# Performance work log

Measured on AMD Instinct MI355X. Metric: run time of the kernel, lower is better.

## Reference

```python
import jax, jax.numpy as jnp
import numpy as np

B, T, C = 2, 2048, 1024
H = 16
HD = C // H  # head_dim = 64


def setup_inputs() -> dict:
    key = jax.random.key(0)
    ks = jax.random.split(key, 5)
    s = 0.02
    return {
        "x": jax.random.normal(ks[0], (B, T, C), dtype=jnp.float32),
        "Wqkv": jax.random.normal(ks[1], (C, 3 * C), dtype=jnp.float32) * s,
        "bqkv": jax.random.normal(ks[2], (3 * C,), dtype=jnp.float32) * s,
        "Wproj": jax.random.normal(ks[3], (C, C), dtype=jnp.float32) * s,
        "bproj": jax.random.normal(ks[4], (C,), dtype=jnp.float32) * s,
    }


def reference(x, Wqkv, bqkv, Wproj, bproj):
    b, t, c = x.shape
    qkv = x @ Wqkv + bqkv  # [B,T,3C]
    q, k, v = jnp.split(qkv, 3, axis=-1)
    # [B,T,C] -> [B,H,T,HD]
    q = q.reshape(b, t, H, HD).transpose(0, 2, 1, 3)
    k = k.reshape(b, t, H, HD).transpose(0, 2, 1, 3)
    v = v.reshape(b, t, H, HD).transpose(0, 2, 1, 3)
    scale = 1.0 / jnp.sqrt(jnp.float32(HD))
    att = jnp.einsum('bhqd,bhkd->bhqk', q, k) * scale  # [B,H,T,T]
    causal = jnp.tril(jnp.ones((t, t), dtype=bool))
    att = jnp.where(causal[None, None], att, jnp.float32(-jnp.inf))
    att = jax.nn.softmax(att, axis=-1)
    y = jnp.einsum('bhqk,bhkd->bhqd', att, v)  # [B,H,T,HD]
    y = y.transpose(0, 2, 1, 3).reshape(b, t, c)
    return y @ Wproj + bproj
```

## Files before the change

### kernel.cpp

```cpp
#include <hip/hip_runtime.h>

typedef unsigned short u16;
typedef __attribute__((ext_vector_type(4))) float f32x4;
typedef __attribute__((ext_vector_type(8))) short short8;

#define AS1 __attribute__((address_space(1)))
#define AS3 __attribute__((address_space(3)))

#define B_  2
#define T_  2048
#define C_  1024
#define H_  16
#define HD_ 64
#define N3C 3072
#define BT_ 4096

__device__ __forceinline__ u16 f2bf(float x) {
    unsigned u = __float_as_uint(x);
    u += 0x7fff + ((u >> 16) & 1);
    return (u16)(u >> 16);
}

__device__ __forceinline__ unsigned cvt_pk_bf16(float a, float b) {
    unsigned r;
    asm("v_cvt_pk_bf16_f32 %0, %1, %2" : "=v"(r) : "v"(a), "v"(b));
    return r;
}

__global__ __launch_bounds__(256)
void conv_all(const float* __restrict__ x, u16* __restrict__ xb,
              const float* __restrict__ Wq, u16* __restrict__ WqT,
              const float* __restrict__ Wp, u16* __restrict__ WpT) {
    __shared__ float tile[64][68];
    const int tid = threadIdx.x;
    const int b = blockIdx.x;
    if (b < 4096) {
        int i = b * 256 + tid;
        float4 f = ((const float4*)x)[i];
        uint2 o;
        o.x = cvt_pk_bf16(f.x, f.y);
        o.y = cvt_pk_bf16(f.z, f.w);
        ((uint2*)xb)[i] = o;
        return;
    }
    const float* W; u16* WT; int N, k0, n0;
    if (b < 4096 + 768) {
        int bb = b - 4096; W = Wq; WT = WqT; N = N3C;
        n0 = (bb % 48) * 64; k0 = (bb / 48) * 64;
    } else {
        int bb = b - 4864; W = Wp; WT = WpT; N = C_;
        n0 = (bb % 16) * 64; k0 = (bb / 16) * 64;
    }
    #pragma unroll
    for (int i = 0; i < 4; ++i) {
        int slot = tid + i * 256;
        int row = slot >> 4, c4 = (slot & 15) * 4;
        *(float4*)&tile[row][c4] = *(const float4*)&W[(size_t)(k0 + row) * N + n0 + c4];
    }
    __syncthreads();
    #pragma unroll
    for (int i = 0; i < 4; ++i) {
        int slot = tid + i * 256;
        int nn = slot >> 4, k4 = (slot & 15) * 4;
        uint2 o;
        o.x = cvt_pk_bf16(tile[k4 + 0][nn], tile[k4 + 1][nn]);
        o.y = cvt_pk_bf16(tile[k4 + 2][nn], tile[k4 + 3][nn]);
        *(uint2*)&WT[(size_t)(n0 + nn) * 1024 + k0 + k4] = o;
    }
}

__device__ __forceinline__ void gemm_core(const u16* __restrict__ A, const u16* __restrict__ BT,
                                          u16* As, u16* Bs,
                                          int m0, int n0, f32x4 (&acc)[4][4]) {
    const int tid = threadIdx.x;
    const int lane = tid & 63, w = tid >> 6;
    const int l15 = lane & 15, quad = lane >> 4;
    const int row0 = (w >> 1) * 64, col0 = (w & 1) * 64;
    const int srow = lane >> 3;
    const int schunk = (lane & 7) ^ srow;

    auto stage = [&](int buf, int k0) {
        #pragma unroll
        for (int j = 0; j < 4; ++j) {
            int rbase = w * 32 + j * 8;
            const u16* ga = A  + (size_t)(m0 + rbase + srow) * 1024 + k0 + schunk * 8;
            const u16* gb = BT + (size_t)(n0 + rbase + srow) * 1024 + k0 + schunk * 8;
            __builtin_amdgcn_global_load_lds((const AS1 void*)ga,
                (AS3 void*)(As + buf * (128 * 64) + rbase * 64), 16, 0, 0);
            __builtin_amdgcn_global_load_lds((const AS1 void*)gb,
                (AS3 void*)(Bs + buf * (128 * 64) + rbase * 64), 16, 0, 0);
        }
    };

    stage(0, 0);
    #pragma unroll
    for (int it = 0; it < 16; ++it) {
        const int cur = it & 1;
        if (it + 1 < 16) {
            stage(cur ^ 1, (it + 1) * 64);
            asm volatile("s_waitcnt vmcnt(8)\n\ts_barrier" ::: "memory");
        } else {
            asm volatile("s_waitcnt vmcnt(0)\n\ts_barrier" ::: "memory");
        }
        const u16* Ac = As + cur * (128 * 64);
        const u16* Bc = Bs + cur * (128 * 64);
        #pragma unroll
        for (int s = 0; s < 2; ++s) {
            short8 a[4], b[4];
            #pragma unroll
            for (int rt = 0; rt < 4; ++rt) {
                int row = row0 + rt * 16 + l15;
                a[rt] = *(const short8*)&Ac[row * 64 + (((s * 4 + quad) ^ (l15 & 7)) * 8)];
            }
            #pragma unroll
            for (int ct = 0; ct < 4; ++ct) {
                int row = col0 + ct * 16 + l15;
                b[ct] = *(const short8*)&Bc[row * 64 + (((s * 4 + quad) ^ (l15 & 7)) * 8)];
            }
            #pragma unroll
            for (int rt = 0; rt < 4; ++rt)
                #pragma unroll
                for (int ct = 0; ct < 4; ++ct)
                    acc[rt][ct] = __builtin_amdgcn_mfma_f32_16x16x32_bf16(a[rt], b[ct], acc[rt][ct], 0, 0, 0);
        }
        asm volatile("s_waitcnt lgkmcnt(0)\n\ts_barrier" ::: "memory");
    }
}

__global__ __launch_bounds__(256)
void qkv_gemm(const u16* __restrict__ A, const u16* __restrict__ BT,
              const float* __restrict__ bias,
              u16* __restrict__ q, u16* __restrict__ k, u16* __restrict__ vT) {
    __shared__ __align__(16) u16 As[2 * 128 * 64];
    __shared__ __align__(16) u16 Bs[2 * 128 * 64];
    const int m0 = blockIdx.y * 128, n0 = blockIdx.x * 128;
    f32x4 acc[4][4] = {};
    gemm_core(A, BT, As, Bs, m0, n0, acc);

    const int tid = threadIdx.x;
    const int lane = tid & 63, w = tid >> 6;
    const int l15 = lane & 15, quad = lane >> 4;
    const int row0 = (w >> 1) * 64, col0 = (w & 1) * 64;
    const int which = n0 >> 10;
    const float QSCALE = 0.125f * 1.4426950408889634f;

    #pragma unroll
    for (int ct = 0; ct < 4; ++ct) {
        int n = n0 + col0 + ct * 16 + l15;
        int nl = n & 1023, h = nl >> 6, d = nl & 63;
        float bv = bias[n];
        #pragma unroll
        for (int rt = 0; rt < 4; ++rt) {
            int mb = m0 + row0 + rt * 16 + quad * 4;
            int bb = mb >> 11, t0 = mb & 2047;
            f32x4 v4 = acc[rt][ct];
            if (which == 0) {
                size_t base = ((size_t)(bb * H_ + h) * T_ + t0) * HD_ + d;
                #pragma unroll
                for (int r = 0; r < 4; ++r)
                    q[base + (size_t)r * HD_] = f2bf((v4[r] + bv) * QSCALE);
            } else if (which == 1) {
                size_t base = ((size_t)(bb * H_ + h) * T_ + t0) * HD_ + d;
                #pragma unroll
                for (int r = 0; r < 4; ++r)
                    k[base + (size_t)r * HD_] = f2bf(v4[r] + bv);
            } else {
                uint2 o;
                o.x = cvt_pk_bf16(v4[0] + bv, v4[1] + bv);
                o.y = cvt_pk_bf16(v4[2] + bv, v4[3] + bv);
                *(uint2*)&vT[((size_t)(bb * H_ + h) * HD_ + d) * T_ + t0] = o;
            }
        }
    }
}

__global__ __launch_bounds__(256, 4)
void attn(const u16* __restrict__ q, const u16* __restrict__ k,
          const u16* __restrict__ vT, u16* __restrict__ y) {
    __shared__ __align__(16) u16 Ks[2 * 64 * 64];
    __shared__ __align__(16) u16 Vs[2 * 64 * 64];
    const int tid = threadIdx.x;
    const int lane = tid & 63, w = tid >> 6;
    const int l15 = lane & 15, quad = lane >> 4;
    const int srow = lane >> 3, schunk = (lane & 7) ^ srow;
    const int idx = blockIdx.x;
    const int bh = idx & 31;
    const int qt = 31 - (idx >> 5);
    const u16* qp = q  + (size_t)bh * T_ * HD_;
    const u16* kp = k  + (size_t)bh * T_ * HD_;
    const u16* vp = vT + (size_t)bh * HD_ * T_;

    const int qrow = qt * 64 + w * 16 + l15;
    short8 qf[2];
    #pragma unroll
    for (int s = 0; s < 2; ++s)
        qf[s] = *(const short8*)&qp[(size_t)qrow * HD_ + s * 32 + quad * 8];

    auto stage = [&](int buf, int kt) {
        const int kb = kt * 64;
        asm volatile("s_waitcnt lgkmcnt(0)" ::: "memory");
        #pragma unroll
        for (int j = 0; j < 2; ++j) {
            int row = w * 16 + j * 8 + srow;
            __builtin_amdgcn_global_load_lds(
                (const AS1 void*)(kp + (size_t)(kb + row) * HD_ + schunk * 8),
                (AS3 void*)(Ks + buf * (64 * 64) + (w * 16 + j * 8) * 64), 16, 0, 0);
            __builtin_amdgcn_global_load_lds(
                (const AS1 void*)(vp + (size_t)row * T_ + kb + schunk * 8),
                (AS3 void*)(Vs + buf * (64 * 64) + (w * 16 + j * 8) * 64), 16, 0, 0);
        }
    };

    f32x4 o[4] = {};
    float l = 0.f;
    stage(0, 0);

    for (int kt = 0; kt <= qt; ++kt) {
        const int kb = kt * 64;
        const int cur = kt & 1;
        if (kt < qt) {
            stage(cur ^ 1, kt + 1);
            asm volatile("s_waitcnt vmcnt(4)\n\ts_barrier" ::: "memory");
        } else {
            asm volatile("s_waitcnt vmcnt(0)\n\ts_barrier" ::: "memory");
        }
        u16* Kc = Ks + cur * (64 * 64);
        const u16* Vc = Vs + cur * (64 * 64);

        short8 ka[4][2], va[4][2];
        #pragma unroll
        for (int ct = 0; ct < 4; ++ct)
            #pragma unroll
            for (int s = 0; s < 2; ++s) {
                int xo = ((s * 4 + quad) ^ (l15 & 7)) * 8;
                ka[ct][s] = *(const short8*)&Kc[(ct * 16 + l15) * 64 + xo];
                va[ct][s] = *(const short8*)&Vc[(ct * 16 + l15) * 64 + xo];
            }
        asm volatile("s_waitcnt lgkmcnt(0)\n\ts_barrier" ::: "memory");

        f32x4 st[4] = {};
        #pragma unroll
        for (int s = 0; s < 2; ++s)
            #pragma unroll
            for (int ct = 0; ct < 4; ++ct)
                st[ct] = __builtin_amdgcn_mfma_f32_16x16x32_bf16(ka[ct][s], qf[s], st[ct], 0, 0, 0);

        float pe[16];
        #pragma unroll
        for (int ct = 0; ct < 4; ++ct)
            #pragma unroll
            for (int r = 0; r < 4; ++r)
                pe[ct * 4 + r] = exp2f(st[ct][r]);
        if (kt == qt) {
            #pragma unroll
            for (int ct = 0; ct < 4; ++ct)
                #pragma unroll
                for (int r = 0; r < 4; ++r)
                    if ((kb + ct * 16 + quad * 4 + r) > qrow) pe[ct * 4 + r] = 0.f;
        }
        float psum = 0.f;
        #pragma unroll
        for (int i = 0; i < 16; ++i) psum += pe[i];
        l += psum;

        u16* Pw = Kc + (w * 16 + l15) * 64;
        #pragma unroll
        for (int ct = 0; ct < 4; ++ct) {
            int chunk = ct * 2 + (quad >> 1);
            int off = ((chunk ^ (l15 & 7)) << 3) + (quad & 1) * 4;
            uint2 pk;
            pk.x = cvt_pk_bf16(pe[ct * 4 + 0], pe[ct * 4 + 1]);
            pk.y = cvt_pk_bf16(pe[ct * 4 + 2], pe[ct * 4 + 3]);
            *(uint2*)&Pw[off] = pk;
        }
        asm volatile("s_waitcnt lgkmcnt(0)" ::: "memory");

        #pragma unroll
        for (int s = 0; s < 2; ++s) {
            short8 pb = *(const short8*)&Pw[(((s * 4 + quad) ^ (l15 & 7)) << 3)];
            #pragma unroll
            for (int n = 0; n < 4; ++n)
                o[n] = __builtin_amdgcn_mfma_f32_16x16x32_bf16(va[n][s], pb, o[n], 0, 0, 0);
        }
    }

    l += __shfl_xor(l, 16); l += __shfl_xor(l, 32);
    const float inv = 1.f / l;
    const int bb = bh >> 4, h = bh & 15;
    #pragma unroll
    for (int n = 0; n < 4; ++n) {
        uint2 pk;
        pk.x = cvt_pk_bf16(o[n][0] * inv, o[n][1] * inv);
        pk.y = cvt_pk_bf16(o[n][2] * inv, o[n][3] * inv);
        *(uint2*)&y[((size_t)(bb * T_ + qrow)) * C_ + h * 64 + n * 16 + quad * 4] = pk;
    }
}

__global__ __launch_bounds__(256, 3)
void proj_gemm(const u16* __restrict__ A, const u16* __restrict__ BT,
               const float* __restrict__ bias, float* __restrict__ out) {
    __shared__ __align__(16) u16 As[2 * 128 * 64];
    __shared__ __align__(16) u16 Bs[2 * 64 * 64];
    const int m0 = blockIdx.y * 128, n0 = blockIdx.x * 64;
    const int tid = threadIdx.x;
    const int lane = tid & 63, w = tid >> 6;
    const int l15 = lane & 15, quad = lane >> 4;
    const int row0 = (w & 1) * 64, col0 = (w >> 1) * 32;
    const int srow = lane >> 3;
    const int schunk = (lane & 7) ^ srow;
    f32x4 acc[4][2] = {};

    auto stage = [&](int buf, int k0) {
        #pragma unroll
        for (int j = 0; j < 4; ++j) {
            int rbase = w * 32 + j * 8;
            const u16* ga = A + (size_t)(m0 + rbase + srow) * 1024 + k0 + schunk * 8;
            __builtin_amdgcn_global_load_lds((const AS1 void*)ga,
                (AS3 void*)(As + buf * (128 * 64) + rbase * 64), 16, 0, 0);
        }
        #pragma unroll
        for (int j = 0; j < 2; ++j) {
            int rbase = w * 16 + j * 8;
            const u16* gb = BT + (size_t)(n0 + rbase + srow) * 1024 + k0 + schunk * 8;
            __builtin_amdgcn_global_load_lds((const AS1 void*)gb,
                (AS3 void*)(Bs + buf * (64 * 64) + rbase * 64), 16, 0, 0);
        }
    };

    stage(0, 0);
    #pragma unroll
    for (int it = 0; it < 16; ++it) {
        const int cur = it & 1;
        if (it + 1 < 16) {
            stage(cur ^ 1, (it + 1) * 64);
            asm volatile("s_waitcnt vmcnt(6)\n\ts_barrier" ::: "memory");
        } else {
            asm volatile("s_waitcnt vmcnt(0)\n\ts_barrier" ::: "memory");
        }
        const u16* Ac = As + cur * (128 * 64);
        const u16* Bc = Bs + cur * (64 * 64);
        #pragma unroll
        for (int s = 0; s < 2; ++s) {
            short8 a[4], b[2];
            #pragma unroll
            for (int rt = 0; rt < 4; ++rt) {
                int row = row0 + rt * 16 + l15;
                a[rt] = *(const short8*)&Ac[row * 64 + (((s * 4 + quad) ^ (l15 & 7)) * 8)];
            }
            #pragma unroll
            for (int ct = 0; ct < 2; ++ct) {
                int row = col0 + ct * 16 + l15;
                b[ct] = *(const short8*)&Bc[row * 64 + (((s * 4 + quad) ^ (l15 & 7)) * 8)];
            }
            #pragma unroll
            for (int rt = 0; rt < 4; ++rt)
                #pragma unroll
                for (int ct = 0; ct < 2; ++ct)
                    acc[rt][ct] = __builtin_amdgcn_mfma_f32_16x16x32_bf16(a[rt], b[ct], acc[rt][ct], 0, 0, 0);
        }
        asm volatile("s_waitcnt lgkmcnt(0)\n\ts_barrier" ::: "memory");
    }

    #pragma unroll
    for (int ct = 0; ct < 2; ++ct) {
        int n = n0 + col0 + ct * 16 + l15;
        float bv = bias[n];
        #pragma unroll
        for (int rt = 0; rt < 4; ++rt) {
            int mb = m0 + row0 + rt * 16 + quad * 4;
            f32x4 v4 = acc[rt][ct];
            #pragma unroll
            for (int r = 0; r < 4; ++r)
                out[(size_t)(mb + r) * 1024 + n] = v4[r] + bv;
        }
    }
}

extern "C" void kernel_launch(void* const* d_in, const int* in_sizes, int n_in,
                              void* d_out, int out_size, void* d_ws, size_t ws_size,
                              hipStream_t stream) {
    const float* x     = (const float*)d_in[0];
    const float* Wqkv  = (const float*)d_in[1];
    const float* bqkv  = (const float*)d_in[2];
    const float* Wproj = (const float*)d_in[3];
    const float* bproj = (const float*)d_in[4];

    u16* xb     = (u16*)d_ws;
    u16* WqkvT  = xb + (size_t)4 * 1024 * 1024;
    u16* WprojT = WqkvT + (size_t)3 * 1024 * 1024;
    u16* q      = WprojT + (size_t)1024 * 1024;
    u16* kk     = q + (size_t)4 * 1024 * 1024;
    u16* vT     = kk + (size_t)4 * 1024 * 1024;
    u16* y      = vT + (size_t)4 * 1024 * 1024;

    conv_all<<<5120, 256, 0, stream>>>(x, xb, Wqkv, WqkvT, Wproj, WprojT);
    qkv_gemm<<<dim3(N3C / 128, BT_ / 128), 256, 0, stream>>>(xb, WqkvT, bqkv, q, kk, vT);
    attn<<<1024, 256, 0, stream>>>(q, kk, vT, y);
    proj_gemm<<<dim3(C_ / 64, BT_ / 128), 256, 0, stream>>>(y, WprojT, bproj, (float*)d_out);
}
```

Baseline: 179.7 us.

## Rewrite QKV GEMM with 256x256 tiles and a four-stage pipelined K loop

```diff
diff --git a/kernel.cpp b/kernel.cpp
--- a/kernel.cpp
+++ b/kernel.cpp
@@ -69,91 +69,111 @@
     }
 }
 
-__device__ __forceinline__ void gemm_core(const u16* __restrict__ A, const u16* __restrict__ BT,
-                                          u16* As, u16* Bs,
-                                          int m0, int n0, f32x4 (&acc)[4][4]) {
-    const int tid = threadIdx.x;
-    const int lane = tid & 63, w = tid >> 6;
-    const int l15 = lane & 15, quad = lane >> 4;
-    const int row0 = (w >> 1) * 64, col0 = (w & 1) * 64;
-    const int srow = lane >> 3;
-    const int schunk = (lane & 7) ^ srow;
-
-    auto stage = [&](int buf, int k0) {
-        #pragma unroll
-        for (int j = 0; j < 4; ++j) {
-            int rbase = w * 32 + j * 8;
-            const u16* ga = A  + (size_t)(m0 + rbase + srow) * 1024 + k0 + schunk * 8;
-            const u16* gb = BT + (size_t)(n0 + rbase + srow) * 1024 + k0 + schunk * 8;
-            __builtin_amdgcn_global_load_lds((const AS1 void*)ga,
-                (AS3 void*)(As + buf * (128 * 64) + rbase * 64), 16, 0, 0);
-            __builtin_amdgcn_global_load_lds((const AS1 void*)gb,
-                (AS3 void*)(Bs + buf * (128 * 64) + rbase * 64), 16, 0, 0);
-        }
-    };
-
-    stage(0, 0);
-    #pragma unroll
-    for (int it = 0; it < 16; ++it) {
-        const int cur = it & 1;
-        if (it + 1 < 16) {
-            stage(cur ^ 1, (it + 1) * 64);
-            asm volatile("s_waitcnt vmcnt(8)\n\ts_barrier" ::: "memory");
-        } else {
-            asm volatile("s_waitcnt vmcnt(0)\n\ts_barrier" ::: "memory");
-        }
-        const u16* Ac = As + cur * (128 * 64);
-        const u16* Bc = Bs + cur * (128 * 64);
-        #pragma unroll
-        for (int s = 0; s < 2; ++s) {
-            short8 a[4], b[4];
-            #pragma unroll
-            for (int rt = 0; rt < 4; ++rt) {
-                int row = row0 + rt * 16 + l15;
-                a[rt] = *(const short8*)&Ac[row * 64 + (((s * 4 + quad) ^ (l15 & 7)) * 8)];
-            }
-            #pragma unroll
-            for (int ct = 0; ct < 4; ++ct) {
-                int row = col0 + ct * 16 + l15;
-                b[ct] = *(const short8*)&Bc[row * 64 + (((s * 4 + quad) ^ (l15 & 7)) * 8)];
-            }
-            #pragma unroll
-            for (int rt = 0; rt < 4; ++rt)
-                #pragma unroll
-                for (int ct = 0; ct < 4; ++ct)
-                    acc[rt][ct] = __builtin_amdgcn_mfma_f32_16x16x32_bf16(a[rt], b[ct], acc[rt][ct], 0, 0, 0);
-        }
-        asm volatile("s_waitcnt lgkmcnt(0)\n\ts_barrier" ::: "memory");
-    }
-}
-
-__global__ __launch_bounds__(256)
+__global__ __launch_bounds__(512, 2)
 void qkv_gemm(const u16* __restrict__ A, const u16* __restrict__ BT,
               const float* __restrict__ bias,
               u16* __restrict__ q, u16* __restrict__ k, u16* __restrict__ vT) {
-    __shared__ __align__(16) u16 As[2 * 128 * 64];
-    __shared__ __align__(16) u16 Bs[2 * 128 * 64];
-    const int m0 = blockIdx.y * 128, n0 = blockIdx.x * 128;
-    f32x4 acc[4][4] = {};
-    gemm_core(A, BT, As, Bs, m0, n0, acc);
-
-    const int tid = threadIdx.x;
+    __shared__ __align__(16) u16 As[4][256 * 32];
+    __shared__ __align__(16) u16 Bs[4][256 * 32];
+    const int tid  = threadIdx.x;
     const int lane = tid & 63, w = tid >> 6;
+    const int wr = w >> 2, wc = w & 3;
     const int l15 = lane & 15, quad = lane >> 4;
-    const int row0 = (w >> 1) * 64, col0 = (w & 1) * 64;
+
+    const int bid = blockIdx.x;
+    const int bm = ((bid & 7) << 1) | ((bid >> 3) & 1);
+    const int bn = bid >> 4;
+    const int m0 = bm * 256, n0 = bn * 256;
+
+    const int srow4 = lane >> 2;
+    const int gch   = ((lane & 3) ^ ((lane >> 2) & 3) ^ (lane >> 4)) * 8;
+    const int fl    = (l15 & 3) ^ (l15 >> 2);
+
+    const u16* gA = A  + (size_t)(m0 + w * 16 + srow4) * 1024 + gch;
+    const u16* gB = BT + (size_t)(n0 + w * 16 + srow4) * 1024 + gch;
+
+    auto stageA = [&](int t) {
+        const int sl = t & 3;
+        #pragma unroll
+        for (int j = 0; j < 2; ++j)
+            __builtin_amdgcn_global_load_lds(
+                (const AS1 void*)(gA + (size_t)j * 128 * 1024 + t * 32),
+                (AS3 void*)(&As[sl][(j * 128 + w * 16) * 32]), 16, 0, 0);
+    };
+    auto stageB = [&](int t) {
+        const int sl = t & 3;
+        #pragma unroll
+        for (int j = 0; j < 2; ++j)
+            __builtin_amdgcn_global_load_lds(
+                (const AS1 void*)(gB + (size_t)j * 128 * 1024 + t * 32),
+                (AS3 void*)(&Bs[sl][(j * 128 + w * 16) * 32]), 16, 0, 0);
+    };
+
+    f32x4 acc[8][4] = {};
+
+    stageA(0); stageB(0); stageA(1); stageB(1); stageA(2); stageB(2);
+    asm volatile("s_waitcnt vmcnt(8)\n\ts_barrier" ::: "memory");
+
+    const int aoff = (wr * 128 + l15) * 32 + (quad ^ fl) * 8;
+    const int boff = (wc * 64  + l15) * 32 + (quad ^ fl) * 8;
+
+    auto tile_body = [&](int t, bool doStage) {
+        const u16* Ac = &As[t & 3][0];
+        const u16* Bc = &Bs[t & 3][0];
+        short8 a[8], b[4];
+        #pragma unroll
+        for (int mf = 0; mf < 4; ++mf)
+            a[mf] = *(const short8*)&Ac[aoff + mf * 512];
+        #pragma unroll
+        for (int nf = 0; nf < 4; ++nf)
+            b[nf] = *(const short8*)&Bc[boff + nf * 512];
+        if (doStage) stageA(t + 3);
+        asm volatile("s_barrier\n\ts_waitcnt lgkmcnt(0)" ::: "memory");
+        __builtin_amdgcn_s_setprio(1);
+        #pragma unroll
+        for (int mf = 0; mf < 4; ++mf)
+            #pragma unroll
+            for (int nf = 0; nf < 4; ++nf)
+                acc[mf][nf] = __builtin_amdgcn_mfma_f32_16x16x32_bf16(a[mf], b[nf], acc[mf][nf], 0, 0, 0);
+        __builtin_amdgcn_s_setprio(0);
+        asm volatile("s_barrier" ::: "memory");
+        #pragma unroll
+        for (int mf = 0; mf < 4; ++mf)
+            a[4 + mf] = *(const short8*)&Ac[aoff + (4 + mf) * 512];
+        if (doStage) stageB(t + 3);
+        asm volatile("s_barrier\n\ts_waitcnt lgkmcnt(0)" ::: "memory");
+        __builtin_amdgcn_s_setprio(1);
+        #pragma unroll
+        for (int mf = 0; mf < 4; ++mf)
+            #pragma unroll
+            for (int nf = 0; nf < 4; ++nf)
+                acc[4 + mf][nf] = __builtin_amdgcn_mfma_f32_16x16x32_bf16(a[4 + mf], b[nf], acc[4 + mf][nf], 0, 0, 0);
+        __builtin_amdgcn_s_setprio(0);
+    };
+
+    #pragma unroll 1
+    for (int t = 0; t < 29; ++t) {
+        tile_body(t, true);
+        asm volatile("s_waitcnt vmcnt(8)\n\ts_barrier" ::: "memory");
+    }
+    tile_body(29, false);
+    asm volatile("s_waitcnt vmcnt(4)\n\ts_barrier" ::: "memory");
+    tile_body(30, false);
+    asm volatile("s_waitcnt vmcnt(0)\n\ts_barrier" ::: "memory");
+    tile_body(31, false);
+
     const int which = n0 >> 10;
     const float QSCALE = 0.125f * 1.4426950408889634f;
-
-    #pragma unroll
-    for (int ct = 0; ct < 4; ++ct) {
-        int n = n0 + col0 + ct * 16 + l15;
-        int nl = n & 1023, h = nl >> 6, d = nl & 63;
-        float bv = bias[n];
-        #pragma unroll
-        for (int rt = 0; rt < 4; ++rt) {
-            int mb = m0 + row0 + rt * 16 + quad * 4;
-            int bb = mb >> 11, t0 = mb & 2047;
-            f32x4 v4 = acc[rt][ct];
+    #pragma unroll
+    for (int nf = 0; nf < 4; ++nf) {
+        const int n = n0 + wc * 64 + nf * 16 + l15;
+        const int nl = n & 1023, h = nl >> 6, d = nl & 63;
+        const float bv = bias[n];
+        #pragma unroll
+        for (int mf = 0; mf < 8; ++mf) {
+            const int mb = m0 + wr * 128 + mf * 16 + quad * 4;
+            const int bb = mb >> 11, t0 = mb & 2047;
+            f32x4 v4 = acc[mf][nf];
             if (which == 0) {
                 size_t base = ((size_t)(bb * H_ + h) * T_ + t0) * HD_ + d;
                 #pragma unroll
@@ -394,7 +414,7 @@
     u16* y      = vT + (size_t)4 * 1024 * 1024;
 
     conv_all<<<5120, 256, 0, stream>>>(x, xb, Wqkv, WqkvT, Wproj, WprojT);
-    qkv_gemm<<<dim3(N3C / 128, BT_ / 128), 256, 0, stream>>>(xb, WqkvT, bqkv, q, kk, vT);
+    qkv_gemm<<<192, 512, 0, stream>>>(xb, WqkvT, bqkv, q, kk, vT);
     attn<<<1024, 256, 0, stream>>>(q, kk, vT, y);
     proj_gemm<<<dim3(C_ / 64, BT_ / 128), 256, 0, stream>>>(y, WprojT, bproj, (float*)d_out);
 }
```

Measured after the change: 188.3 us. 1.05x slower.
